# Kernel optimization log

Hardware: AMD Instinct MI355X
Metric: run time of the kernel (lower is better)

## Reference

```python
import jax, jax.numpy as jnp
import numpy as np

TEMP = 0.5
WEIGHT = (0.4, 0.3, 0.3)


def _l2norm(x):
    n = jnp.linalg.norm(x, axis=-1, keepdims=True)
    return x / jnp.maximum(n, 1e-12)


def _forward(st_i, st_j, car_i, car_j, pl_i, pl_j, gt_labels,
             cen_st, cen_car, cen_pl, conc):
    w = jnp.asarray(WEIGHT, dtype=st_i.dtype)[:, None, None]  # [3,1,1]
    feats = [jnp.concatenate([_l2norm(a), _l2norm(b)], axis=0)
             for a, b in ((st_i, st_j), (car_i, car_j), (pl_i, pl_j))]  # each [N,D]
    sims = jnp.stack([f @ f.T for f in feats])  # [3,N,N]
    wmask = jnp.where(sims == 0, jnp.zeros_like(w), w)
    wsim = (sims * wmask).sum(0) / (wmask.sum(0) + 1e-12)  # [N,N]
    e = jnp.exp(wsim / TEMP)
    N = e.shape[0]
    B = N // 2
    idx = jnp.arange(N)
    pos = e[idx, (idx + B) % N]  # positive_mask gather: one positive per row
    # negative_mask excludes diagonal and the positive -> row sum minus both
    neg_sum = e.sum(-1) - e[idx, idx] - pos
    loss = (-jnp.log(pos / (pos + neg_sum))).mean()

    # prototype branch: gt_labels covers all C clusters, unique set == arange(C)
    labels = gt_labels[:, 0]  # [N]
    C = cen_st.shape[0]
    k = jnp.arange(C - 1)
    neg_ids = k[None, :] + (k[None, :] >= labels[:, None]).astype(k.dtype)  # sorted ids != label
    proto_ids = jnp.concatenate([labels[:, None], neg_ids], axis=1)  # [N,C], col 0 = positive
    logits = jnp.stack([
        jnp.take_along_axis(f @ c.T, proto_ids, axis=1)
        for f, c in zip(feats, (cen_st, cen_car, cen_pl))])  # [3,N,C]
    temp_proto = conc[:, proto_ids]  # [3,N,C]
    logits = logits / (temp_proto + 1e-12)
    w2 = jnp.where((temp_proto == 0) | (logits == 0), jnp.zeros_like(w), w)
    logits_w = (logits * w2).sum(0) / (w2.sum(0) + 1e-12)  # [N,C]
    # CrossEntropyLoss(mean) with target class 0 for every row
    loss_proto = (-jax.nn.log_softmax(logits_w, axis=-1)[:, 0]).mean()
    return loss + loss_proto


def setup_inputs() -> dict:
    key = jax.random.key(0)
    ks = jax.random.split(key, 12)
    B, D, C = 2048, 128, 512
    N = 2 * B
    inp = {}
    names = ['st_feat_i', 'st_feat_j', 'car_feat_i', 'car_feat_j',
             'plate_feat_i', 'plate_feat_j']
    for i, nm in enumerate(names):
        inp[nm] = jax.random.normal(ks[i], (B, D), dtype=jnp.float32)
    # labels covering all C clusters so torch.unique(gt_labels) == arange(C)
    labels = jnp.tile(jnp.arange(C, dtype=jnp.int32), N // C)
    labels = jax.random.permutation(ks[6], labels)
    inp['gt_labels'] = labels[:, None]
    inp['st_centroids'] = jax.random.normal(ks[7], (C, D), dtype=jnp.float32)
    inp['car_centroids'] = jax.random.normal(ks[8], (C, D), dtype=jnp.float32)
    inp['plate_centroids'] = jax.random.normal(ks[9], (C, D), dtype=jnp.float32)
    inp['concentration'] = jax.random.uniform(ks[10], (3, C), dtype=jnp.float32,
                                              minval=0.1, maxval=1.0)
    return inp


def reference(st_feat_i, st_feat_j, car_feat_i, car_feat_j,
              plate_feat_i, plate_feat_j, gt_labels,
              st_centroids, car_centroids, plate_centroids, concentration):
    return _forward(st_feat_i, st_feat_j, car_feat_i, car_feat_j,
                    plate_feat_i, plate_feat_j, gt_labels,
                    st_centroids, car_centroids, plate_centroids, concentration)
```

## Files before the change

### kernel.cpp

```cpp
#include <hip/hip_runtime.h>
#include <hip/hip_bf16.h>
#include <math.h>

#define BB 2048
#define NN 4096
#define DD 128
#define CC 512
#define NSIM 528
#define NPROTO 128

typedef __attribute__((ext_vector_type(8))) short bf16x8;
typedef __attribute__((ext_vector_type(4))) float f32x4;

#define LDS_PTR(p) ((__attribute__((address_space(3))) uint32_t*)(p))
#define GLB_PTR(p) ((const __attribute__((address_space(1))) uint32_t*)(p))

__global__ __launch_bounds__(512) void k_normprep(
    const float* __restrict__ si, const float* __restrict__ sj,
    const float* __restrict__ ci, const float* __restrict__ cj,
    const float* __restrict__ pi, const float* __restrict__ pj,
    const float* __restrict__ cst, const float* __restrict__ cca,
    const float* __restrict__ cpl, const float* __restrict__ conc,
    __hip_bfloat16* __restrict__ fbf, __hip_bfloat16* __restrict__ cbf,
    float* __restrict__ rowsum) {
  const int tid = threadIdx.x;
  const int w   = tid >> 6;
  const int t   = tid & 63;

  if (blockIdx.x < 2) {
    const int i = (blockIdx.x * 512 + tid) * 4;
    *(float4*)(rowsum + i) = make_float4(0.f, 0.f, 0.f, 0.f);
  }

  if (blockIdx.x < NN / 8) {
    const int row = blockIdx.x * 8 + w;
    const int r = (row < BB) ? row : row - BB;
    #pragma unroll
    for (int m = 0; m < 3; ++m) {
      const float* src;
      if (m == 0)      src = (row < BB) ? si : sj;
      else if (m == 1) src = (row < BB) ? ci : cj;
      else             src = (row < BB) ? pi : pj;
      const float sqw = (m == 0) ? 0.632455532033676f : 0.547722557505166f;
      float2 v = ((const float2*)(src + (size_t)r * DD))[t];
      float ss = v.x * v.x + v.y * v.y;
      #pragma unroll
      for (int k = 32; k >= 1; k >>= 1) ss += __shfl_xor(ss, k);
      const float inv = sqw / fmaxf(sqrtf(ss), 1e-12f);
      __hip_bfloat16* db = fbf + (size_t)m * NN * DD + (size_t)row * DD;
      db[2 * t]     = __float2bfloat16(v.x * inv);
      db[2 * t + 1] = __float2bfloat16(v.y * inv);
    }
  } else {
    const int crow = (blockIdx.x - NN / 8) * 8 + w;
    #pragma unroll
    for (int m = 0; m < 3; ++m) {
      const float* src = (m == 0) ? cst : (m == 1) ? cca : cpl;
      const float sqw = (m == 0) ? 0.632455532033676f : 0.547722557505166f;
      const float sc = sqw / (conc[m * CC + crow] + 1e-12f);
      float2 v = ((const float2*)(src + (size_t)crow * DD))[t];
      __hip_bfloat16* db = cbf + (size_t)m * CC * DD + (size_t)crow * DD;
      db[2 * t]     = __float2bfloat16(v.x * sc);
      db[2 * t + 1] = __float2bfloat16(v.y * sc);
    }
  }
}

__global__ __launch_bounds__(256, 3) void k_main(const __hip_bfloat16* __restrict__ fbf,
                                                 const __hip_bfloat16* __restrict__ cbf,
                                                 const int* __restrict__ labels,
                                                 float* __restrict__ rowsum,
                                                 float* __restrict__ pos_e,
                                                 float* __restrict__ diag_e,
                                                 float* __restrict__ pmax_g,
                                                 float* __restrict__ psum_g,
                                                 float* __restrict__ zl_g) {
  __shared__ bf16x8 As[1024];
  __shared__ bf16x8 Bs[1024];

  const int tid  = threadIdx.x;
  const int lane = tid & 63;
  const int wid  = tid >> 6;
  const int l15  = lane & 15;
  const int kg   = lane >> 4;

  if (blockIdx.x < NSIM) {
    int tB = blockIdx.x;
    int by = 0;
    while (tB >= 32 - by) { tB -= 32 - by; ++by; }
    const int bx = by + tB;
    const bool diag = (by == bx);
    const int rowBase = by * 128;
    const int colBase = bx * 128;

    const int wr = wid >> 1, wc = wid & 1;
    const int rl = lane >> 3;
    const int kc = (lane & 7) ^ rl;

    f32x4 acc[4][4] = {};

    for (int t = 0; t < 6; ++t) {
      const __hip_bfloat16* F = fbf + (size_t)(t >> 1) * NN * DD + (t & 1) * 64;
      #pragma unroll
      for (int q = 0; q < 4; ++q) {
        const int row = q * 32 + wid * 8 + rl;
        __builtin_amdgcn_global_load_lds(
            GLB_PTR(F + (size_t)(rowBase + row) * DD + kc * 8),
            LDS_PTR(&As[q * 256 + wid * 64]), 16, 0, 0);
        if (!diag)
          __builtin_amdgcn_global_load_lds(
              GLB_PTR(F + (size_t)(colBase + row) * DD + kc * 8),
              LDS_PTR(&Bs[q * 256 + wid * 64]), 16, 0, 0);
      }
      __syncthreads();

      const bf16x8* Bsrc = diag ? As : Bs;
      #pragma unroll
      for (int ks2 = 0; ks2 < 2; ++ks2) {
        bf16x8 a[4], b[4];
        const int ch = (ks2 * 4 + kg) ^ (l15 & 7);
        #pragma unroll
        for (int ti = 0; ti < 4; ++ti)
          a[ti] = As[(wr * 64 + ti * 16 + l15) * 8 + ch];
        #pragma unroll
        for (int tj = 0; tj < 4; ++tj)
          b[tj] = Bsrc[(wc * 64 + tj * 16 + l15) * 8 + ch];
        #pragma unroll
        for (int ti = 0; ti < 4; ++ti)
          #pragma unroll
          for (int tj = 0; tj < 4; ++tj)
            acc[ti][tj] = __builtin_amdgcn_mfma_f32_16x16x32_bf16(a[ti], b[tj], acc[ti][tj], 0, 0, 0);
      }
      if (t < 5) __syncthreads();
    }

    float csum[4] = {0.f, 0.f, 0.f, 0.f};
    #pragma unroll
    for (int ti = 0; ti < 4; ++ti) {
      #pragma unroll
      for (int j = 0; j < 4; ++j) {
        const int i = rowBase + wr * 64 + ti * 16 + kg * 4 + j;
        float rsum = 0.f;
        #pragma unroll
        for (int tj = 0; tj < 4; ++tj) {
          const int jcol = colBase + wc * 64 + tj * 16 + l15;
          const float e = __expf(2.0f * acc[ti][tj][j]);
          rsum += e;
          csum[tj] += e;
          if (diag) {
            if (jcol == i) diag_e[i] = e;
          } else if (jcol == ((i + BB) & (NN - 1))) {
            pos_e[i] = e;
            pos_e[jcol] = e;
          }
        }
        #pragma unroll
        for (int msk = 8; msk >= 1; msk >>= 1) rsum += __shfl_xor(rsum, msk);
        if (l15 == 0) atomicAdd(&rowsum[i], rsum);
      }
    }
    if (!diag) {
      #pragma unroll
      for (int tj = 0; tj < 4; ++tj) {
        float v = csum[tj];
        v += __shfl_xor(v, 16);
        v += __shfl_xor(v, 32);
        if (lane < 16) atomicAdd(&rowsum[colBase + wc * 64 + tj * 16 + l15], v);
      }
    }
  } else {
    float* wmaxs = (float*)As;
    float* wsums = wmaxs + 256;
    int*   slab  = (int*)(wsums + 256);

    const int bidp = blockIdx.x - NSIM;
    const int half = bidp & 1;
    const int row0 = (bidp >> 1) * 64;
    const int cbase = half * 256 + wid * 64;

    if (tid < 64) slab[tid] = labels[row0 + tid];
    __syncthreads();

    f32x4 acc[4][4] = {};
    #pragma unroll
    for (int ks = 0; ks < 12; ++ks) {
      const int koff = (ks & 3) * 32 + kg * 8;
      const __hip_bfloat16* F  = fbf + (size_t)(ks >> 2) * NN * DD + koff;
      const __hip_bfloat16* Cm = cbf + (size_t)(ks >> 2) * CC * DD + koff;
      bf16x8 af[4], bfr[4];
      #pragma unroll
      for (int ti = 0; ti < 4; ++ti)
        af[ti] = *(const bf16x8*)(F + (size_t)(row0 + ti * 16 + l15) * DD);
      #pragma unroll
      for (int tj = 0; tj < 4; ++tj)
        bfr[tj] = *(const bf16x8*)(Cm + (size_t)(cbase + tj * 16 + l15) * DD);
      #pragma unroll
      for (int ti = 0; ti < 4; ++ti)
        #pragma unroll
        for (int tj = 0; tj < 4; ++tj)
          acc[ti][tj] = __builtin_amdgcn_mfma_f32_16x16x32_bf16(af[ti], bfr[tj], acc[ti][tj], 0, 0, 0);
    }

    #pragma unroll
    for (int ti = 0; ti < 4; ++ti) {
      #pragma unroll
      for (int j = 0; j < 4; ++j) {
        const int r = ti * 16 + kg * 4 + j;
        #pragma unroll
        for (int tj = 0; tj < 4; ++tj) {
          const int c = cbase + tj * 16 + l15;
          if (c == slab[r]) zl_g[row0 + r] = acc[ti][tj][j];
        }
      }
    }

    #pragma unroll
    for (int ti = 0; ti < 4; ++ti) {
      #pragma unroll
      for (int j = 0; j < 4; ++j) {
        const int r = ti * 16 + kg * 4 + j;
        float mx = acc[ti][0][j];
        #pragma unroll
        for (int tj = 1; tj < 4; ++tj) mx = fmaxf(mx, acc[ti][tj][j]);
        #pragma unroll
        for (int msk = 8; msk >= 1; msk >>= 1) mx = fmaxf(mx, __shfl_xor(mx, msk));
        if (l15 == 0) wmaxs[wid * 64 + r] = mx;
      }
    }
    __syncthreads();

    #pragma unroll
    for (int ti = 0; ti < 4; ++ti) {
      #pragma unroll
      for (int j = 0; j < 4; ++j) {
        const int r = ti * 16 + kg * 4 + j;
        const float bmx = fmaxf(fmaxf(wmaxs[0 * 64 + r], wmaxs[1 * 64 + r]),
                                fmaxf(wmaxs[2 * 64 + r], wmaxs[3 * 64 + r]));
        float se = 0.f;
        #pragma unroll
        for (int tj = 0; tj < 4; ++tj) se += __expf(acc[ti][tj][j] - bmx);
        #pragma unroll
        for (int msk = 8; msk >= 1; msk >>= 1) se += __shfl_xor(se, msk);
        if (l15 == 0) wsums[wid * 64 + r] = se;
      }
    }
    __syncthreads();

    if (tid < 64) {
      const int r = tid;
      const float bmx = fmaxf(fmaxf(wmaxs[0 * 64 + r], wmaxs[1 * 64 + r]),
                              fmaxf(wmaxs[2 * 64 + r], wmaxs[3 * 64 + r]));
      const float s = wsums[0 * 64 + r] + wsums[1 * 64 + r] +
                      wsums[2 * 64 + r] + wsums[3 * 64 + r];
      pmax_g[(size_t)half * NN + row0 + r] = bmx;
      psum_g[(size_t)half * NN + row0 + r] = s;
    }
  }
}

__global__ void k_final(const float* __restrict__ rowsum, const float* __restrict__ pos_e,
                        const float* __restrict__ diag_e, const float* __restrict__ pmax_g,
                        const float* __restrict__ psum_g, const float* __restrict__ zl_g,
                        float* __restrict__ out) {
  __shared__ float redA[4], redB[4];
  const int tid = threadIdx.x;
  float sa = 0.f, sb = 0.f;
  for (int i = tid; i < NN; i += 256) {
    sa += __logf(rowsum[i] - diag_e[i]) - __logf(pos_e[i]);
    const float m0 = pmax_g[i], m1 = pmax_g[NN + i];
    const float M = fmaxf(m0, m1);
    const float s = psum_g[i] * __expf(m0 - M) + psum_g[NN + i] * __expf(m1 - M);
    sb += M + __logf(s) - zl_g[i];
  }
  const int lane = tid & 63, wv = tid >> 6;
  #pragma unroll
  for (int k = 32; k >= 1; k >>= 1) { sa += __shfl_xor(sa, k); sb += __shfl_xor(sb, k); }
  if (lane == 0) { redA[wv] = sa; redB[wv] = sb; }
  __syncthreads();
  if (tid == 0) {
    const float la = redA[0] + redA[1] + redA[2] + redA[3];
    const float lb = redB[0] + redB[1] + redB[2] + redB[3];
    out[0] = la / (float)NN + lb / (float)NN;
  }
}

extern "C" void kernel_launch(void* const* d_in, const int* in_sizes, int n_in,
                              void* d_out, int out_size, void* d_ws, size_t ws_size,
                              hipStream_t stream) {
  (void)in_sizes; (void)n_in; (void)out_size; (void)ws_size;
  const float* si  = (const float*)d_in[0];
  const float* sj  = (const float*)d_in[1];
  const float* ci  = (const float*)d_in[2];
  const float* cj  = (const float*)d_in[3];
  const float* pi  = (const float*)d_in[4];
  const float* pj  = (const float*)d_in[5];
  const int*   lab = (const int*)d_in[6];
  const float* cst = (const float*)d_in[7];
  const float* cca = (const float*)d_in[8];
  const float* cpl = (const float*)d_in[9];
  const float* cnc = (const float*)d_in[10];

  float* ws     = (float*)d_ws;
  float* rowsum = ws;
  float* pos_e  = rowsum + NN;
  float* diag_e = pos_e + NN;
  float* pmax_g = diag_e + NN;
  float* psum_g = pmax_g + 2 * NN;
  float* zl_g   = psum_g + 2 * NN;
  __hip_bfloat16* fbf = (__hip_bfloat16*)(zl_g + NN);
  __hip_bfloat16* cbf = fbf + (size_t)3 * NN * DD;

  k_normprep<<<NN / 8 + CC / 8, 512, 0, stream>>>(si, sj, ci, cj, pi, pj,
                                                  cst, cca, cpl, cnc, fbf, cbf, rowsum);
  k_main<<<NSIM + NPROTO, 256, 0, stream>>>(fbf, cbf, lab, rowsum, pos_e, diag_e,
                                            pmax_g, psum_g, zl_g);
  k_final<<<1, 256, 0, stream>>>(rowsum, pos_e, diag_e, pmax_g, psum_g, zl_g, (float*)d_out);
}
```

Before: 119.0 us.

## Double-buffer LDS tiles in similarity GEMM to overlap loads with MFMA

Splits the As/Bs shared-memory tiles into two buffers and issues the global-to-LDS load for the next K-stage before computing on the current one, so memory latency overlaps with MFMA work. It also removes one barrier per iteration. LDS use per block doubles to 64 KB, and the launch-bounds occupancy hint is lowered from 3 to 2 blocks per CU, which may cut latency hiding across blocks.

```diff
diff --git a/kernel.cpp b/kernel.cpp
--- a/kernel.cpp
+++ b/kernel.cpp
@@ -66,7 +66,7 @@
   }
 }
 
-__global__ __launch_bounds__(256, 3) void k_main(const __hip_bfloat16* __restrict__ fbf,
+__global__ __launch_bounds__(256, 2) void k_main(const __hip_bfloat16* __restrict__ fbf,
                                                  const __hip_bfloat16* __restrict__ cbf,
                                                  const int* __restrict__ labels,
                                                  float* __restrict__ rowsum,
@@ -75,8 +75,8 @@
                                                  float* __restrict__ pmax_g,
                                                  float* __restrict__ psum_g,
                                                  float* __restrict__ zl_g) {
-  __shared__ bf16x8 As[1024];
-  __shared__ bf16x8 Bs[1024];
+  __shared__ bf16x8 As[2][1024];
+  __shared__ bf16x8 Bs[2][1024];
 
   const int tid  = threadIdx.x;
   const int lane = tid & 63;
@@ -99,29 +99,38 @@
 
     f32x4 acc[4][4] = {};
 
+    #define STAGE(t_, buf_)                                                          \
+      do {                                                                           \
+        const __hip_bfloat16* F_ = fbf + (size_t)((t_) >> 1) * NN * DD + ((t_) & 1) * 64; \
+        _Pragma("unroll")                                                            \
+        for (int q = 0; q < 4; ++q) {                                                \
+          const int row_ = q * 32 + wid * 8 + rl;                                    \
+          __builtin_amdgcn_global_load_lds(                                          \
+              GLB_PTR(F_ + (size_t)(rowBase + row_) * DD + kc * 8),                  \
+              LDS_PTR(&As[buf_][q * 256 + wid * 64]), 16, 0, 0);                     \
+          if (!diag)                                                                 \
+            __builtin_amdgcn_global_load_lds(                                        \
+                GLB_PTR(F_ + (size_t)(colBase + row_) * DD + kc * 8),                \
+                LDS_PTR(&Bs[buf_][q * 256 + wid * 64]), 16, 0, 0);                   \
+        }                                                                            \
+      } while (0)
+
+    STAGE(0, 0);
+    __syncthreads();
+
+    int cur = 0;
     for (int t = 0; t < 6; ++t) {
-      const __hip_bfloat16* F = fbf + (size_t)(t >> 1) * NN * DD + (t & 1) * 64;
-      #pragma unroll
-      for (int q = 0; q < 4; ++q) {
-        const int row = q * 32 + wid * 8 + rl;
-        __builtin_amdgcn_global_load_lds(
-            GLB_PTR(F + (size_t)(rowBase + row) * DD + kc * 8),
-            LDS_PTR(&As[q * 256 + wid * 64]), 16, 0, 0);
-        if (!diag)
-          __builtin_amdgcn_global_load_lds(
-              GLB_PTR(F + (size_t)(colBase + row) * DD + kc * 8),
-              LDS_PTR(&Bs[q * 256 + wid * 64]), 16, 0, 0);
-      }
-      __syncthreads();
-
-      const bf16x8* Bsrc = diag ? As : Bs;
+      if (t < 5) STAGE(t + 1, cur ^ 1);
+
+      const bf16x8* Asrc = As[cur];
+      const bf16x8* Bsrc = diag ? As[cur] : Bs[cur];
       #pragma unroll
       for (int ks2 = 0; ks2 < 2; ++ks2) {
         bf16x8 a[4], b[4];
         const int ch = (ks2 * 4 + kg) ^ (l15 & 7);
         #pragma unroll
         for (int ti = 0; ti < 4; ++ti)
-          a[ti] = As[(wr * 64 + ti * 16 + l15) * 8 + ch];
+          a[ti] = Asrc[(wr * 64 + ti * 16 + l15) * 8 + ch];
         #pragma unroll
         for (int tj = 0; tj < 4; ++tj)
           b[tj] = Bsrc[(wc * 64 + tj * 16 + l15) * 8 + ch];
@@ -131,8 +140,10 @@
           for (int tj = 0; tj < 4; ++tj)
             acc[ti][tj] = __builtin_amdgcn_mfma_f32_16x16x32_bf16(a[ti], b[tj], acc[ti][tj], 0, 0, 0);
       }
-      if (t < 5) __syncthreads();
-    }
+      __syncthreads();
+      cur ^= 1;
+    }
+    #undef STAGE
 
     float csum[4] = {0.f, 0.f, 0.f, 0.f};
     #pragma unroll
@@ -169,7 +180,7 @@
       }
     }
   } else {
-    float* wmaxs = (float*)As;
+    float* wmaxs = (float*)&As[0][0];
     float* wsums = wmaxs + 256;
     int*   slab  = (int*)(wsums + 256);
 
```

Result: slower. 132.0 us (+10.9%).
